# Performance work log

Measured on AMD Instinct MI355X. Metric: run time of the kernel, lower is better.

## Reference

```python
import jax, jax.numpy as jnp
import numpy as np

NUM_NODES = 1_000_000
HIDDEN_DIM = 128
NUM_GRAPHS = 4096
EPS = 1e-05


def setup_inputs() -> dict:
    key = jax.random.key(0)
    kx, kb = jax.random.split(key)
    x = jax.random.normal(kx, (NUM_NODES, HIDDEN_DIM), dtype=jnp.float32)
    batch = jnp.sort(jax.random.randint(kb, (NUM_NODES,), 0, NUM_GRAPHS)).astype(jnp.int64)
    weight = jnp.ones((HIDDEN_DIM,), dtype=jnp.float32)
    bias = jnp.zeros((HIDDEN_DIM,), dtype=jnp.float32)
    return {"x": x, "batch": batch, "weight": weight, "bias": bias}


def reference(x, batch, weight, bias):
    # Single-pass segment reduction replacing the torch per-graph python loop.
    seg = batch.astype(jnp.int32)
    cnt = jax.ops.segment_sum(jnp.ones((x.shape[0],), x.dtype), seg,
                              num_segments=NUM_GRAPHS)            # [G]
    s = jax.ops.segment_sum(x, seg, num_segments=NUM_GRAPHS)      # [G, D]
    sq = jax.ops.segment_sum(x * x, seg, num_segments=NUM_GRAPHS) # [G, D]
    safe = jnp.maximum(cnt, 1.0)[:, None]
    mean = s / safe
    var = sq / safe - mean * mean                                 # unbiased=False
    # torch code leaves the initial (mean=0, var=1) for segments with <=1 node
    ok = (cnt > 1.0)[:, None]
    mean = jnp.where(ok, mean, 0.0)
    var = jnp.where(ok, var, 1.0)
    mu = mean[seg]   # [N, D] per-node gather (matches broadcasted torch.where)
    v = var[seg]     # [N, D]
    normalized = (x - mu) / jnp.sqrt(v + EPS)
    return weight * normalized + bias
```

## Files before the change

kernel.cpp:

```cpp
#include <hip/hip_runtime.h>

#define NUM_GRAPHS 4096
#define DV 32
#define EPS 1e-5f

__global__ __launch_bounds__(256) void graphnorm_kernel(
    const float* __restrict__ x,
    const int*   __restrict__ batch,
    const float* __restrict__ weight,
    const float* __restrict__ bias,
    float*       __restrict__ out,
    int n_nodes)
{
    const int g = blockIdx.x;
    const int t = threadIdx.x;
    const int c = t & 31;
    const int r = t >> 5;

    int lo = 0, hi = n_nodes;
    while (lo < hi) { int m = (lo + hi) >> 1; if (batch[m] < g) lo = m + 1; else hi = m; }
    const int start = lo;
    hi = n_nodes;
    while (lo < hi) { int m = (lo + hi) >> 1; if (batch[m] < g + 1) lo = m + 1; else hi = m; }
    const int end = lo;
    const int cnt = end - start;
    if (cnt == 0) return;

    __shared__ float4 red_s[256];
    __shared__ float4 red_q[256];
    __shared__ float4 sm_a[32];
    __shared__ float4 sm_c[32];

    const float4* __restrict__ xr = (const float4*)x + (size_t)start * DV;
    float4*       __restrict__ orr = (float4*)out + (size_t)start * DV;

    float4 s = make_float4(0.f, 0.f, 0.f, 0.f);
    float4 q = make_float4(0.f, 0.f, 0.f, 0.f);
    for (int i = r; i < cnt; i += 8) {
        float4 v = xr[(size_t)i * DV + c];
        s.x += v.x; s.y += v.y; s.z += v.z; s.w += v.w;
        q.x += v.x * v.x; q.y += v.y * v.y; q.z += v.z * v.z; q.w += v.w * v.w;
    }
    red_s[t] = s;
    red_q[t] = q;
    __syncthreads();

    if (t < 32) {
        float4 S = red_s[t], Q = red_q[t];
        #pragma unroll
        for (int j = 1; j < 8; ++j) {
            float4 a = red_s[t + 32 * j];
            float4 b2 = red_q[t + 32 * j];
            S.x += a.x;  S.y += a.y;  S.z += a.z;  S.w += a.w;
            Q.x += b2.x; Q.y += b2.y; Q.z += b2.z; Q.w += b2.w;
        }
        float4 mean, var, inv;
        if (cnt > 1) {
            const float ic = 1.0f / (float)cnt;
            mean.x = S.x * ic; mean.y = S.y * ic; mean.z = S.z * ic; mean.w = S.w * ic;
            var.x = fmaf(-mean.x, mean.x, Q.x * ic);
            var.y = fmaf(-mean.y, mean.y, Q.y * ic);
            var.z = fmaf(-mean.z, mean.z, Q.z * ic);
            var.w = fmaf(-mean.w, mean.w, Q.w * ic);
        } else {
            mean = make_float4(0.f, 0.f, 0.f, 0.f);
            var  = make_float4(1.f, 1.f, 1.f, 1.f);
        }
        inv.x = rsqrtf(var.x + EPS);
        inv.y = rsqrtf(var.y + EPS);
        inv.z = rsqrtf(var.z + EPS);
        inv.w = rsqrtf(var.w + EPS);

        float4 w4 = ((const float4*)weight)[t];
        float4 b4 = ((const float4*)bias)[t];
        float4 A, C;
        A.x = w4.x * inv.x; A.y = w4.y * inv.y; A.z = w4.z * inv.z; A.w = w4.w * inv.w;
        C.x = fmaf(-mean.x, A.x, b4.x);
        C.y = fmaf(-mean.y, A.y, b4.y);
        C.z = fmaf(-mean.z, A.z, b4.z);
        C.w = fmaf(-mean.w, A.w, b4.w);
        sm_a[t] = A;
        sm_c[t] = C;
    }
    __syncthreads();

    const float4 A = sm_a[c];
    const float4 C = sm_c[c];
    for (int i = r; i < cnt; i += 8) {
        float4 v = xr[(size_t)i * DV + c];
        float4 o;
        o.x = fmaf(v.x, A.x, C.x);
        o.y = fmaf(v.y, A.y, C.y);
        o.z = fmaf(v.z, A.z, C.z);
        o.w = fmaf(v.w, A.w, C.w);
        orr[(size_t)i * DV + c] = o;
    }
}

extern "C" void kernel_launch(void* const* d_in, const int* in_sizes, int n_in,
                              void* d_out, int out_size, void* d_ws, size_t ws_size,
                              hipStream_t stream) {
    const float* x      = (const float*)d_in[0];
    const int*   batch  = (const int*)d_in[1];
    const float* weight = (const float*)d_in[2];
    const float* bias   = (const float*)d_in[3];
    float*       out    = (float*)d_out;
    const int n_nodes = in_sizes[1];

    graphnorm_kernel<<<NUM_GRAPHS, 256, 0, stream>>>(x, batch, weight, bias, out, n_nodes);
}
```

Baseline: 916.6 us.

## Cache segment rows in registers, precompute boundaries, use nontemporal access

Each thread now keeps up to 36 float4 rows of its segment in registers, so the normalize pass reuses them instead of reading x from memory a second time. A separate pre-kernel computes segment start offsets into the workspace, replacing the per-block binary searches. Loads and stores use nontemporal builtins. The large register array forces launch_bounds(256,2) and can lower occupancy or cause spills, and the extra kernel launch scans the whole batch array.

```diff
diff --git a/kernel.cpp b/kernel.cpp
--- a/kernel.cpp
+++ b/kernel.cpp
@@ -3,10 +3,27 @@
 #define NUM_GRAPHS 4096
 #define DV 32
 #define EPS 1e-5f
+#define RK 36
 
-__global__ __launch_bounds__(256) void graphnorm_kernel(
+typedef float f32x4 __attribute__((ext_vector_type(4)));
+
+__global__ __launch_bounds__(256) void boundaries_kernel(
+    const int* __restrict__ batch, int* __restrict__ starts, int n)
+{
+    int i = blockIdx.x * blockDim.x + threadIdx.x;
+    if (i >= n) return;
+    int b0 = batch[i];
+    int b1 = (i + 1 < n) ? batch[i + 1] : NUM_GRAPHS;
+    if (i == 0) {
+        for (int g = 0; g <= b0; ++g) starts[g] = 0;
+    }
+    for (int g = b0 + 1; g <= b1; ++g) starts[g] = i + 1;
+}
+
+__global__ __launch_bounds__(256, 2) void graphnorm_kernel(
     const float* __restrict__ x,
     const int*   __restrict__ batch,
+    const int*   __restrict__ starts,
     const float* __restrict__ weight,
     const float* __restrict__ bias,
     float*       __restrict__ out,
@@ -17,64 +34,84 @@
     const int c = t & 31;
     const int r = t >> 5;
 
-    int lo = 0, hi = n_nodes;
-    while (lo < hi) { int m = (lo + hi) >> 1; if (batch[m] < g) lo = m + 1; else hi = m; }
-    const int start = lo;
-    hi = n_nodes;
-    while (lo < hi) { int m = (lo + hi) >> 1; if (batch[m] < g + 1) lo = m + 1; else hi = m; }
-    const int end = lo;
+    int start, end;
+    if (starts != nullptr) {
+        start = starts[g];
+        end   = starts[g + 1];
+    } else {
+        int lo = 0, hi = n_nodes;
+        while (lo < hi) { int m = (lo + hi) >> 1; if (batch[m] < g) lo = m + 1; else hi = m; }
+        start = lo;
+        hi = n_nodes;
+        while (lo < hi) { int m = (lo + hi) >> 1; if (batch[m] < g + 1) lo = m + 1; else hi = m; }
+        end = lo;
+    }
     const int cnt = end - start;
     if (cnt == 0) return;
 
-    __shared__ float4 red_s[256];
-    __shared__ float4 red_q[256];
-    __shared__ float4 sm_a[32];
-    __shared__ float4 sm_c[32];
+    __shared__ f32x4 red_s[256];
+    __shared__ f32x4 red_q[256];
+    __shared__ f32x4 sm_a[32];
+    __shared__ f32x4 sm_c[32];
 
-    const float4* __restrict__ xr = (const float4*)x + (size_t)start * DV;
-    float4*       __restrict__ orr = (float4*)out + (size_t)start * DV;
+    const f32x4* __restrict__ xr  = (const f32x4*)x   + (size_t)start * DV + c;
+    f32x4*       __restrict__ orr = (f32x4*)out       + (size_t)start * DV + c;
 
-    float4 s = make_float4(0.f, 0.f, 0.f, 0.f);
-    float4 q = make_float4(0.f, 0.f, 0.f, 0.f);
-    for (int i = r; i < cnt; i += 8) {
-        float4 v = xr[(size_t)i * DV + c];
-        s.x += v.x; s.y += v.y; s.z += v.z; s.w += v.w;
-        q.x += v.x * v.x; q.y += v.y * v.y; q.z += v.z * v.z; q.w += v.w * v.w;
+    f32x4 reg[RK];
+    f32x4 s = {0.f, 0.f, 0.f, 0.f};
+    f32x4 q = {0.f, 0.f, 0.f, 0.f};
+
+    #pragma unroll
+    for (int k = 0; k < RK; ++k) {
+        const int i = r + 8 * k;
+        if (i < cnt) reg[k] = __builtin_nontemporal_load(xr + (size_t)i * DV);
     }
+    #pragma unroll
+    for (int k = 0; k < RK; ++k) {
+        const int i = r + 8 * k;
+        if (i < cnt) {
+            f32x4 v = reg[k];
+            s += v;
+            q += v * v;
+        }
+    }
+    for (int i = r + 8 * RK; i < cnt; i += 8) {
+        f32x4 v = xr[(size_t)i * DV];
+        s += v;
+        q += v * v;
+    }
+
     red_s[t] = s;
     red_q[t] = q;
     __syncthreads();
 
     if (t < 32) {
-        float4 S = red_s[t], Q = red_q[t];
+        f32x4 S = red_s[t], Q = red_q[t];
         #pragma unroll
         for (int j = 1; j < 8; ++j) {
-            float4 a = red_s[t + 32 * j];
-            float4 b2 = red_q[t + 32 * j];
-            S.x += a.x;  S.y += a.y;  S.z += a.z;  S.w += a.w;
-            Q.x += b2.x; Q.y += b2.y; Q.z += b2.z; Q.w += b2.w;
+            S += red_s[t + 32 * j];
+            Q += red_q[t + 32 * j];
         }
-        float4 mean, var, inv;
+        f32x4 mean = {0.f, 0.f, 0.f, 0.f};
+        f32x4 var  = {1.f, 1.f, 1.f, 1.f};
         if (cnt > 1) {
             const float ic = 1.0f / (float)cnt;
-            mean.x = S.x * ic; mean.y = S.y * ic; mean.z = S.z * ic; mean.w = S.w * ic;
+            mean = S * ic;
             var.x = fmaf(-mean.x, mean.x, Q.x * ic);
             var.y = fmaf(-mean.y, mean.y, Q.y * ic);
             var.z = fmaf(-mean.z, mean.z, Q.z * ic);
             var.w = fmaf(-mean.w, mean.w, Q.w * ic);
-        } else {
-            mean = make_float4(0.f, 0.f, 0.f, 0.f);
-            var  = make_float4(1.f, 1.f, 1.f, 1.f);
         }
+        f32x4 inv;
         inv.x = rsqrtf(var.x + EPS);
         inv.y = rsqrtf(var.y + EPS);
         inv.z = rsqrtf(var.z + EPS);
         inv.w = rsqrtf(var.w + EPS);
 
-        float4 w4 = ((const float4*)weight)[t];
-        float4 b4 = ((const float4*)bias)[t];
-        float4 A, C;
-        A.x = w4.x * inv.x; A.y = w4.y * inv.y; A.z = w4.z * inv.z; A.w = w4.w * inv.w;
+        f32x4 w4 = ((const f32x4*)weight)[t];
+        f32x4 b4 = ((const f32x4*)bias)[t];
+        f32x4 A = w4 * inv;
+        f32x4 C;
         C.x = fmaf(-mean.x, A.x, b4.x);
         C.y = fmaf(-mean.y, A.y, b4.y);
         C.z = fmaf(-mean.z, A.z, b4.z);
@@ -84,16 +121,29 @@
     }
     __syncthreads();
 
-    const float4 A = sm_a[c];
-    const float4 C = sm_c[c];
-    for (int i = r; i < cnt; i += 8) {
-        float4 v = xr[(size_t)i * DV + c];
-        float4 o;
+    const f32x4 A = sm_a[c];
+    const f32x4 C = sm_c[c];
+    #pragma unroll
+    for (int k = 0; k < RK; ++k) {
+        const int i = r + 8 * k;
+        if (i < cnt) {
+            f32x4 v = reg[k];
+            f32x4 o;
+            o.x = fmaf(v.x, A.x, C.x);
+            o.y = fmaf(v.y, A.y, C.y);
+            o.z = fmaf(v.z, A.z, C.z);
+            o.w = fmaf(v.w, A.w, C.w);
+            __builtin_nontemporal_store(o, orr + (size_t)i * DV);
+        }
+    }
+    for (int i = r + 8 * RK; i < cnt; i += 8) {
+        f32x4 v = xr[(size_t)i * DV];
+        f32x4 o;
         o.x = fmaf(v.x, A.x, C.x);
         o.y = fmaf(v.y, A.y, C.y);
         o.z = fmaf(v.z, A.z, C.z);
         o.w = fmaf(v.w, A.w, C.w);
-        orr[(size_t)i * DV + c] = o;
+        __builtin_nontemporal_store(o, orr + (size_t)i * DV);
     }
 }
 
@@ -107,5 +157,12 @@
     float*       out    = (float*)d_out;
     const int n_nodes = in_sizes[1];
 
-    graphnorm_kernel<<<NUM_GRAPHS, 256, 0, stream>>>(x, batch, weight, bias, out, n_nodes);
+    int* starts = nullptr;
+    if (d_ws != nullptr && ws_size >= (size_t)(NUM_GRAPHS + 1) * sizeof(int)) {
+        starts = (int*)d_ws;
+        int nb = (n_nodes + 255) / 256;
+        boundaries_kernel<<<nb, 256, 0, stream>>>(batch, starts, n_nodes);
+    }
+    graphnorm_kernel<<<NUM_GRAPHS, 256, 0, stream>>>(
+        x, batch, starts, weight, bias, out, n_nodes);
 }
```

New measurement: 801.5 us. 12.6% less time.
